# Kernel optimization log

Hardware: AMD Instinct MI355X
Metric: run time of the kernel (lower is better)

## Reference

```python
import jax, jax.numpy as jnp
import numpy as np

NUM_EXPERTS = 8
HIDDEN = 1024
INTERMEDIATE = 2816
TOTAL_TOKENS = 4096  # 512 tokens per expert


def setup_inputs() -> dict:
    key = jax.random.key(0)
    k_x, k1, k2, k3 = jax.random.split(key, 4)
    hiddens = jax.random.normal(k_x, (TOTAL_TOKENS, HIDDEN), dtype=jnp.float32)
    # tokens assumed pre-sorted by expert; equal-sized groups here
    batch_sizes = jnp.full((NUM_EXPERTS,), TOTAL_TOKENS // NUM_EXPERTS, dtype=jnp.int64)
    w1_weight = jax.random.normal(k1, (NUM_EXPERTS, HIDDEN, INTERMEDIATE), dtype=jnp.float32)
    w2_weight = jax.random.normal(k2, (NUM_EXPERTS, INTERMEDIATE, HIDDEN), dtype=jnp.float32)
    w3_weight = jax.random.normal(k3, (NUM_EXPERTS, HIDDEN, INTERMEDIATE), dtype=jnp.float32)
    return {
        "hiddens": hiddens,
        "w1_weight": w1_weight,
        "w2_weight": w2_weight,
        "w3_weight": w3_weight,
        "batch_sizes": batch_sizes,
    }


def _grouped_moe(hiddens, w1, w2, w3, batch_sizes):
    """Grouped SwiGLU FFN: tokens are contiguous per expert (sizes = batch_sizes).

    Jit-safe formulation: map each token to its expert id, then run one masked
    dense GEMM trio per expert (small fixed expert count). Zero rows contribute
    exactly zero (silu(0)*0 == 0), so no final masking of the output is needed.
    """
    num_experts = w1.shape[0]
    total_tokens = hiddens.shape[0]
    bounds = jnp.cumsum(batch_sizes)  # [E] exclusive-right boundaries
    expert_ids = jnp.searchsorted(bounds, jnp.arange(total_tokens), side="right")  # [T]
    out = jnp.zeros((total_tokens, w2.shape[-1]), dtype=hiddens.dtype)
    for e in range(num_experts):
        mask = (expert_ids == e)[:, None]  # [T, 1]
        xe = jnp.where(mask, hiddens, 0)   # zero out other experts' tokens
        up = jax.nn.silu(xe @ w1[e]) * (xe @ w3[e])  # [T, F] SwiGLU
        out = out + up @ w2[e]             # [T, H]
    return out


def reference(hiddens, w1_weight, w2_weight, w3_weight, batch_sizes):
    return _grouped_moe(hiddens, w1_weight, w2_weight, w3_weight, batch_sizes)
```

## Files before the change

### kernel.cpp

```cpp
#include <hip/hip_runtime.h>
#include <hip/hip_bf16.h>

#define NE 8
#define HD 1024
#define ID 2816
#define TT 4096
#define BM 128
#define BK 32
#define BN1 64
#define BN2 64
#define MAXMT (TT / BM + NE)
#define NKS1 (HD / BK)
#define NKS2 (ID / BK)
#define ATILE 8192

typedef __attribute__((ext_vector_type(4))) float f32x4;
typedef __attribute__((ext_vector_type(8))) short s16x8;
typedef __attribute__((ext_vector_type(4))) int i32x4;

__device__ __forceinline__ unsigned int f2bfpk(float lo, float hi) {
  float2 t; t.x = lo; t.y = hi;
  union { __hip_bfloat162 h2; unsigned int u; } cv;
  cv.h2 = __float22bfloat162_rn(t);
  return cv.u;
}

__device__ __forceinline__ void lds_barrier() {
  asm volatile("s_waitcnt lgkmcnt(0)" ::: "memory");
  __builtin_amdgcn_s_barrier();
}

__device__ __forceinline__ void glds16(const void* g, void* l) {
  __builtin_amdgcn_global_load_lds(
      (const __attribute__((address_space(1))) void*)g,
      (__attribute__((address_space(3))) void*)l, 16, 0, 0);
}

__device__ __forceinline__ bool map_tile(const void* bsp, int mt, int& e,
                                         int& mstart, int& rowend) {
  const int* w = (const int*)bsp;
  bool is64 = (w[1] == 0) && (w[3] == 0) && (w[5] == 0) && (w[7] == 0) &&
              ((w[0] | w[2] | w[4] | w[6]) != 0);
  long long start = 0;
  int rem = mt;
  for (int i = 0; i < NE; ++i) {
    long long b = is64 ? ((const long long*)bsp)[i] : (long long)w[i];
    if (b < 0) b = 0;
    int tiles = (int)((b + BM - 1) / BM);
    if (rem < tiles) {
      long long m0 = start + (long long)rem * BM;
      long long me = start + b;
      if (m0 >= TT) return false;
      if (me > TT) me = TT;
      e = i; mstart = (int)m0; rowend = (int)me;
      return true;
    }
    rem -= tiles;
    start += b;
  }
  return false;
}

__global__ __launch_bounds__(256) void cvt_xt(const float* __restrict__ x,
                                              const void* __restrict__ bsp,
                                              unsigned short* __restrict__ xt) {
  int mt = blockIdx.x >> 5;
  int ks = blockIdx.x & 31;
  int e, mstart, rowend;
  if (!map_tile(bsp, mt, e, mstart, rowend)) return;
  int t = threadIdx.x;
  int lane = t & 63;
  int r = lane & 15, q = lane >> 4;
  unsigned short* ob = xt + ((size_t)mt * NKS1 + ks) * (ATILE / 2);
#pragma unroll
  for (int h = 0; h < 2; ++h) {
    int f = h * 4 + (t >> 6);
    int row = mstart + f * 16 + r;
    s16x8 o = (s16x8)0;
    if (row < rowend) {
      const float* src = x + (size_t)row * HD + ks * 32 + q * 8;
      f32x4 v0 = *(const f32x4*)src;
      f32x4 v1 = *(const f32x4*)(src + 4);
      unsigned int d0 = f2bfpk(v0[0], v0[1]), d1 = f2bfpk(v0[2], v0[3]);
      unsigned int d2 = f2bfpk(v1[0], v1[1]), d3 = f2bfpk(v1[2], v1[3]);
      o[0] = (short)d0; o[1] = (short)(d0 >> 16);
      o[2] = (short)d1; o[3] = (short)(d1 >> 16);
      o[4] = (short)d2; o[5] = (short)(d2 >> 16);
      o[6] = (short)d3; o[7] = (short)(d3 >> 16);
    }
    *(s16x8*)(ob + h * 2048 + t * 8) = o;
  }
}

__global__ __launch_bounds__(256, 4) void moe_gemm1(
    const unsigned short* __restrict__ xt, const float* __restrict__ w1,
    const float* __restrict__ w3, const void* __restrict__ bsp,
    __hip_bfloat16* __restrict__ up) {
  __shared__ __align__(16) char As[2][ATILE];
  __shared__ __align__(16) char B1s[2][4096];
  __shared__ __align__(16) char B3s[2][4096];

  const int NWG = (ID / BN1) * MAXMT;
  int bid = blockIdx.x;
  int logical = (bid & 7) * (NWG >> 3) + (bid >> 3);
  int mt = logical % MAXMT;
  int nt = logical / MAXMT;
  int e, mstart, rowend;
  if (!map_tile(bsp, mt, e, mstart, rowend)) return;
  const int n0 = nt * BN1;
  const int tid = threadIdx.x;
  const int lane = tid & 63;
  const int wv = tid >> 6;
  const int wr = wv >> 1, wc = wv & 1;
  const int q = lane >> 4, r16 = lane & 15;

  const int b_n = tid & 63, b_kq = tid >> 6;
  const int boff = (b_n >> 4) * 1024 + b_kq * 256 + (b_n & 15) * 16;
  const char* agp = (const char*)xt + (size_t)mt * NKS1 * ATILE + tid * 16;
  const float* w1c = w1 + (size_t)e * HD * ID + (size_t)(8 * b_kq) * ID + n0 + b_n;
  const float* w3c = w3 + (size_t)e * HD * ID + (size_t)(8 * b_kq) * ID + n0 + b_n;

  f32x4 acc1[4][2], acc3[4][2];
#pragma unroll
  for (int i = 0; i < 4; ++i)
#pragma unroll
    for (int j = 0; j < 2; ++j) { acc1[i][j] = (f32x4)0.f; acc3[i][j] = (f32x4)0.f; }

  float Wc1[8], Wc3[8];

  auto gldsA = [&](int k, int buf) {
    const char* s = agp + (size_t)k * ATILE;
    char* d = &As[buf][0] + tid * 16;
    glds16(s, d);
    glds16(s + 4096, d + 4096);
  };
  auto loadB = [&]() {
#pragma unroll
    for (int i = 0; i < 8; ++i) {
      Wc1[i] = w1c[(size_t)i * ID];
      Wc3[i] = w3c[(size_t)i * ID];
    }
    w1c += (size_t)BK * ID; w3c += (size_t)BK * ID;
  };
  auto storeB = [&](int buf) {
    i32x4 p1, p3;
    p1[0] = (int)f2bfpk(Wc1[0], Wc1[1]); p1[1] = (int)f2bfpk(Wc1[2], Wc1[3]);
    p1[2] = (int)f2bfpk(Wc1[4], Wc1[5]); p1[3] = (int)f2bfpk(Wc1[6], Wc1[7]);
    *(i32x4*)(B1s[buf] + boff) = p1;
    p3[0] = (int)f2bfpk(Wc3[0], Wc3[1]); p3[1] = (int)f2bfpk(Wc3[2], Wc3[3]);
    p3[2] = (int)f2bfpk(Wc3[4], Wc3[5]); p3[3] = (int)f2bfpk(Wc3[6], Wc3[7]);
    *(i32x4*)(B3s[buf] + boff) = p3;
  };
  auto compute = [&](int ab, int bb) {
    s16x8 a[4], b1[2], b3[2];
#pragma unroll
    for (int i = 0; i < 4; ++i)
      a[i] = *(const s16x8*)(As[ab] + (wr * 4 + i) * 1024 + lane * 16);
#pragma unroll
    for (int j = 0; j < 2; ++j) {
      b1[j] = *(const s16x8*)(B1s[bb] + (wc * 2 + j) * 1024 + lane * 16);
      b3[j] = *(const s16x8*)(B3s[bb] + (wc * 2 + j) * 1024 + lane * 16);
    }
#pragma unroll
    for (int i = 0; i < 4; ++i)
#pragma unroll
      for (int j = 0; j < 2; ++j) {
        acc1[i][j] = __builtin_amdgcn_mfma_f32_16x16x32_bf16(a[i], b1[j], acc1[i][j], 0, 0, 0);
        acc3[i][j] = __builtin_amdgcn_mfma_f32_16x16x32_bf16(a[i], b3[j], acc3[i][j], 0, 0, 0);
      }
  };

  gldsA(0, 0);
  __builtin_amdgcn_sched_barrier(0);
  loadB();
  storeB(0);
  lds_barrier();
  for (int kt = 0; kt < NKS1; kt += 2) {
    if (kt + 1 < NKS1) {
      gldsA(kt + 1, 1);
      __builtin_amdgcn_sched_barrier(0);
      loadB();
      __builtin_amdgcn_sched_barrier(0);
    }
    compute(0, 0);
    if (kt + 1 < NKS1) { storeB(1); lds_barrier(); }
    if (kt + 2 < NKS1) {
      gldsA(kt + 2, 0);
      __builtin_amdgcn_sched_barrier(0);
      loadB();
      __builtin_amdgcn_sched_barrier(0);
    }
    compute(1, 1);
    if (kt + 2 < NKS1) { storeB(0); lds_barrier(); }
  }

#pragma unroll
  for (int i = 0; i < 4; ++i)
#pragma unroll
    for (int r = 0; r < 4; ++r) {
      int gm = mstart + wr * 64 + i * 16 + q * 4 + r;
      if (gm < rowend) {
#pragma unroll
        for (int j = 0; j < 2; ++j) {
          float v1 = acc1[i][j][r], v3 = acc3[i][j][r];
          float s = v1 / (1.f + __expf(-v1));
          up[(size_t)gm * ID + n0 + wc * 32 + j * 16 + r16] = __float2bfloat16(s * v3);
        }
      }
    }
}

__global__ __launch_bounds__(256, 4) void moe_gemm2(
    const __hip_bfloat16* __restrict__ up, const float* __restrict__ w2,
    const void* __restrict__ bsp, float* __restrict__ out) {
  __shared__ __align__(16) char As[2][ATILE];
  __shared__ __align__(16) char Bs[2][4096];

  const int NWG = (HD / BN2) * MAXMT;
  int bid = blockIdx.x;
  int logical = (bid & 7) * (NWG >> 3) + (bid >> 3);
  int mt = logical % MAXMT;
  int nt = logical / MAXMT;
  int e, mstart, rowend;
  if (!map_tile(bsp, mt, e, mstart, rowend)) return;
  const int n0 = nt * BN2;
  const int tid = threadIdx.x;
  const int lane = tid & 63;
  const int wv = tid >> 6;
  const int wr = wv >> 1, wc = wv & 1;
  const int q = lane >> 4, r16 = lane & 15;

  const int b_n = tid & 63, b_kq = tid >> 6;
  const int boff = (b_n >> 4) * 1024 + b_kq * 256 + (b_n & 15) * 16;
  const float* w2c = w2 + (size_t)e * ID * HD + (size_t)(8 * b_kq) * HD + n0 + b_n;

  int row0 = mstart + (tid >> 6) * 16 + (tid & 15);
  int row1 = row0 + 64;
  row0 = row0 < TT ? row0 : TT - 1;
  row1 = row1 < TT ? row1 : TT - 1;
  const char* uc0 = (const char*)up + ((size_t)row0 * ID + q * 8) * 2;
  const char* uc1 = (const char*)up + ((size_t)row1 * ID + q * 8) * 2;

  f32x4 acc[4][2];
#pragma unroll
  for (int i = 0; i < 4; ++i)
#pragma unroll
    for (int j = 0; j < 2; ++j) acc[i][j] = (f32x4)0.f;

  float Wc[8];

  auto gldsA = [&](int buf) {
    char* d = &As[buf][0] + tid * 16;
    glds16(uc0, d);
    glds16(uc1, d + 4096);
    uc0 += BK * 2; uc1 += BK * 2;
  };
  auto loadB = [&]() {
#pragma unroll
    for (int i = 0; i < 8; ++i) Wc[i] = w2c[(size_t)i * HD];
    w2c += (size_t)BK * HD;
  };
  auto storeB = [&](int buf) {
    i32x4 p;
    p[0] = (int)f2bfpk(Wc[0], Wc[1]); p[1] = (int)f2bfpk(Wc[2], Wc[3]);
    p[2] = (int)f2bfpk(Wc[4], Wc[5]); p[3] = (int)f2bfpk(Wc[6], Wc[7]);
    *(i32x4*)(Bs[buf] + boff) = p;
  };
  auto compute = [&](int ab, int bb) {
    s16x8 a[4], b[2];
#pragma unroll
    for (int i = 0; i < 4; ++i)
      a[i] = *(const s16x8*)(As[ab] + (wr * 4 + i) * 1024 + lane * 16);
#pragma unroll
    for (int j = 0; j < 2; ++j)
      b[j] = *(const s16x8*)(Bs[bb] + (wc * 2 + j) * 1024 + lane * 16);
#pragma unroll
    for (int i = 0; i < 4; ++i)
#pragma unroll
      for (int j = 0; j < 2; ++j)
        acc[i][j] = __builtin_amdgcn_mfma_f32_16x16x32_bf16(a[i], b[j], acc[i][j], 0, 0, 0);
  };

  gldsA(0);
  __builtin_amdgcn_sched_barrier(0);
  loadB();
  storeB(0);
  lds_barrier();
  for (int kt = 0; kt < NKS2; kt += 2) {
    if (kt + 1 < NKS2) {
      gldsA(1);
      __builtin_amdgcn_sched_barrier(0);
      loadB();
      __builtin_amdgcn_sched_barrier(0);
    }
    compute(0, 0);
    if (kt + 1 < NKS2) { storeB(1); lds_barrier(); }
    if (kt + 2 < NKS2) {
      gldsA(0);
      __builtin_amdgcn_sched_barrier(0);
      loadB();
      __builtin_amdgcn_sched_barrier(0);
    }
    compute(1, 1);
    if (kt + 2 < NKS2) { storeB(0); lds_barrier(); }
  }

#pragma unroll
  for (int i = 0; i < 4; ++i)
#pragma unroll
    for (int r = 0; r < 4; ++r) {
      int gm = mstart + wr * 64 + i * 16 + q * 4 + r;
      if (gm < rowend) {
#pragma unroll
        for (int j = 0; j < 2; ++j)
          out[(size_t)gm * HD + n0 + wc * 32 + j * 16 + r16] = acc[i][j][r];
      }
    }
}

extern "C" void kernel_launch(void* const* d_in, const int* in_sizes, int n_in,
                              void* d_out, int out_size, void* d_ws, size_t ws_size,
                              hipStream_t stream) {
  const float* x = (const float*)d_in[0];
  const float* w1 = (const float*)d_in[1];
  const float* w2 = (const float*)d_in[2];
  const float* w3 = (const float*)d_in[3];
  const void* bs = d_in[4];
  float* out = (float*)d_out;
  unsigned short* xt = (unsigned short*)d_ws;
  __hip_bfloat16* up =
      (__hip_bfloat16*)((char*)d_ws + (size_t)MAXMT * NKS1 * ATILE);

  hipMemsetAsync(d_out, 0, (size_t)out_size * sizeof(float), stream);

  cvt_xt<<<dim3(MAXMT * NKS1), dim3(256), 0, stream>>>(x, bs, xt);
  moe_gemm1<<<dim3((ID / BN1) * MAXMT), dim3(256), 0, stream>>>(xt, w1, w3, bs, up);
  moe_gemm2<<<dim3((HD / BN2) * MAXMT), dim3(256), 0, stream>>>(up, w2, bs, out);
}
```

Before: 205.2 us.

## Prefetch weight tiles two stages ahead with register double-buffering and partial vmcnt waits

Both GEMM kernels now keep two register buffers for the fp32 weight tile, so global loads for stage k+2 are issued before computing stage k. Barriers use explicit s_waitcnt vmcnt(N) to wait only for older loads, letting the newest weight loads stay in flight across the barrier. This hides more global-memory latency on the weight stream. The cost is more registers, so gemm1 launch bounds drop from 4 to 3 waves per SIMD, which lowers occupancy, and correctness depends on the hand-counted vmcnt values.

```diff
diff --git a/kernel.cpp b/kernel.cpp
--- a/kernel.cpp
+++ b/kernel.cpp
@@ -23,11 +23,6 @@
   union { __hip_bfloat162 h2; unsigned int u; } cv;
   cv.h2 = __float22bfloat162_rn(t);
   return cv.u;
-}
-
-__device__ __forceinline__ void lds_barrier() {
-  asm volatile("s_waitcnt lgkmcnt(0)" ::: "memory");
-  __builtin_amdgcn_s_barrier();
 }
 
 __device__ __forceinline__ void glds16(const void* g, void* l) {
@@ -92,7 +87,7 @@
   }
 }
 
-__global__ __launch_bounds__(256, 4) void moe_gemm1(
+__global__ __launch_bounds__(256, 3) void moe_gemm1(
     const unsigned short* __restrict__ xt, const float* __restrict__ w1,
     const float* __restrict__ w3, const void* __restrict__ bsp,
     __hip_bfloat16* __restrict__ up) {
@@ -126,7 +121,7 @@
 #pragma unroll
     for (int j = 0; j < 2; ++j) { acc1[i][j] = (f32x4)0.f; acc3[i][j] = (f32x4)0.f; }
 
-  float Wc1[8], Wc3[8];
+  float Wa1[8], Wa3[8], Wb1[8], Wb3[8];
 
   auto gldsA = [&](int k, int buf) {
     const char* s = agp + (size_t)k * ATILE;
@@ -134,21 +129,21 @@
     glds16(s, d);
     glds16(s + 4096, d + 4096);
   };
-  auto loadB = [&]() {
+  auto loadB = [&](float* W1_, float* W3_) {
 #pragma unroll
     for (int i = 0; i < 8; ++i) {
-      Wc1[i] = w1c[(size_t)i * ID];
-      Wc3[i] = w3c[(size_t)i * ID];
+      W1_[i] = w1c[(size_t)i * ID];
+      W3_[i] = w3c[(size_t)i * ID];
     }
     w1c += (size_t)BK * ID; w3c += (size_t)BK * ID;
   };
-  auto storeB = [&](int buf) {
+  auto storeB = [&](int buf, const float* W1_, const float* W3_) {
     i32x4 p1, p3;
-    p1[0] = (int)f2bfpk(Wc1[0], Wc1[1]); p1[1] = (int)f2bfpk(Wc1[2], Wc1[3]);
-    p1[2] = (int)f2bfpk(Wc1[4], Wc1[5]); p1[3] = (int)f2bfpk(Wc1[6], Wc1[7]);
+    p1[0] = (int)f2bfpk(W1_[0], W1_[1]); p1[1] = (int)f2bfpk(W1_[2], W1_[3]);
+    p1[2] = (int)f2bfpk(W1_[4], W1_[5]); p1[3] = (int)f2bfpk(W1_[6], W1_[7]);
     *(i32x4*)(B1s[buf] + boff) = p1;
-    p3[0] = (int)f2bfpk(Wc3[0], Wc3[1]); p3[1] = (int)f2bfpk(Wc3[2], Wc3[3]);
-    p3[2] = (int)f2bfpk(Wc3[4], Wc3[5]); p3[3] = (int)f2bfpk(Wc3[6], Wc3[7]);
+    p3[0] = (int)f2bfpk(W3_[0], W3_[1]); p3[1] = (int)f2bfpk(W3_[2], W3_[3]);
+    p3[2] = (int)f2bfpk(W3_[4], W3_[5]); p3[3] = (int)f2bfpk(W3_[6], W3_[7]);
     *(i32x4*)(B3s[buf] + boff) = p3;
   };
   auto compute = [&](int ab, int bb) {
@@ -170,29 +165,43 @@
       }
   };
 
+#define G1PHASE(P, KC)                                                    \
+  {                                                                       \
+    const bool doG = (kt + (KC) + 1 < NKS1);                              \
+    const bool doL = (kt + (KC) + 2 < NKS1);                              \
+    if (doG) {                                                            \
+      gldsA(kt + (KC) + 1, (P) ^ 1);                                      \
+      __builtin_amdgcn_sched_barrier(0);                                  \
+    }                                                                     \
+    if (doL) {                                                            \
+      loadB((P) ? Wb1 : Wa1, (P) ? Wb3 : Wa3);                            \
+      __builtin_amdgcn_sched_barrier(0);                                  \
+    }                                                                     \
+    compute((P), (P));                                                    \
+    if (doG) {                                                            \
+      storeB((P) ^ 1, (P) ? Wa1 : Wb1, (P) ? Wa3 : Wb3);                  \
+      if (doL)                                                            \
+        asm volatile("s_waitcnt vmcnt(16) lgkmcnt(0)" ::: "memory");      \
+      else                                                                \
+        asm volatile("s_waitcnt vmcnt(0) lgkmcnt(0)" ::: "memory");       \
+      __builtin_amdgcn_s_barrier();                                       \
+    }                                                                     \
+  }
+
   gldsA(0, 0);
   __builtin_amdgcn_sched_barrier(0);
-  loadB();
-  storeB(0);
-  lds_barrier();
+  loadB(Wa1, Wa3);
+  __builtin_amdgcn_sched_barrier(0);
+  loadB(Wb1, Wb3);
+  storeB(0, Wa1, Wa3);
+  asm volatile("s_waitcnt vmcnt(16) lgkmcnt(0)" ::: "memory");
+  __builtin_amdgcn_s_barrier();
+
   for (int kt = 0; kt < NKS1; kt += 2) {
-    if (kt + 1 < NKS1) {
-      gldsA(kt + 1, 1);
-      __builtin_amdgcn_sched_barrier(0);
-      loadB();
-      __builtin_amdgcn_sched_barrier(0);
-    }
-    compute(0, 0);
-    if (kt + 1 < NKS1) { storeB(1); lds_barrier(); }
-    if (kt + 2 < NKS1) {
-      gldsA(kt + 2, 0);
-      __builtin_amdgcn_sched_barrier(0);
-      loadB();
-      __builtin_amdgcn_sched_barrier(0);
-    }
-    compute(1, 1);
-    if (kt + 2 < NKS1) { storeB(0); lds_barrier(); }
-  }
+    G1PHASE(0, 0)
+    G1PHASE(1, 1)
+  }
+#undef G1PHASE
 
 #pragma unroll
   for (int i = 0; i < 4; ++i)
@@ -247,7 +256,7 @@
 #pragma unroll
     for (int j = 0; j < 2; ++j) acc[i][j] = (f32x4)0.f;
 
-  float Wc[8];
+  float Wa[8], Wb[8];
 
   auto gldsA = [&](int buf) {
     char* d = &As[buf][0] + tid * 16;
@@ -255,15 +264,15 @@
     glds16(uc1, d + 4096);
     uc0 += BK * 2; uc1 += BK * 2;
   };
-  auto loadB = [&]() {
-#pragma unroll
-    for (int i = 0; i < 8; ++i) Wc[i] = w2c[(size_t)i * HD];
+  auto loadB = [&](float* W_) {
+#pragma unroll
+    for (int i = 0; i < 8; ++i) W_[i] = w2c[(size_t)i * HD];
     w2c += (size_t)BK * HD;
   };
-  auto storeB = [&](int buf) {
+  auto storeB = [&](int buf, const float* W_) {
     i32x4 p;
-    p[0] = (int)f2bfpk(Wc[0], Wc[1]); p[1] = (int)f2bfpk(Wc[2], Wc[3]);
-    p[2] = (int)f2bfpk(Wc[4], Wc[5]); p[3] = (int)f2bfpk(Wc[6], Wc[7]);
+    p[0] = (int)f2bfpk(W_[0], W_[1]); p[1] = (int)f2bfpk(W_[2], W_[3]);
+    p[2] = (int)f2bfpk(W_[4], W_[5]); p[3] = (int)f2bfpk(W_[6], W_[7]);
     *(i32x4*)(Bs[buf] + boff) = p;
   };
   auto compute = [&](int ab, int bb) {
@@ -281,29 +290,43 @@
         acc[i][j] = __builtin_amdgcn_mfma_f32_16x16x32_bf16(a[i], b[j], acc[i][j], 0, 0, 0);
   };
 
+#define G2PHASE(P, KC)                                                    \
+  {                                                                       \
+    const bool doG = (kt + (KC) + 1 < NKS2);                              \
+    const bool doL = (kt + (KC) + 2 < NKS2);                              \
+    if (doG) {                                                            \
+      gldsA((P) ^ 1);                                                     \
+      __builtin_amdgcn_sched_barrier(0);                                  \
+    }                                                                     \
+    if (doL) {                                                            \
+      loadB((P) ? Wb : Wa);                                               \
+      __builtin_amdgcn_sched_barrier(0);                                  \
+    }                                                                     \
+    compute((P), (P));                                                    \
+    if (doG) {                                                            \
+      storeB((P) ^ 1, (P) ? Wa : Wb);                                     \
+      if (doL)                                                            \
+        asm volatile("s_waitcnt vmcnt(8) lgkmcnt(0)" ::: "memory");       \
+      else                                                                \
+        asm volatile("s_waitcnt vmcnt(0) lgkmcnt(0)" ::: "memory");       \
+      __builtin_amdgcn_s_barrier();                                       \
+    }                                                                     \
+  }
+
   gldsA(0);
   __builtin_amdgcn_sched_barrier(0);
-  loadB();
-  storeB(0);
-  lds_barrier();
+  loadB(Wa);
+  __builtin_amdgcn_sched_barrier(0);
+  loadB(Wb);
+  storeB(0, Wa);
+  asm volatile("s_waitcnt vmcnt(8) lgkmcnt(0)" ::: "memory");
+  __builtin_amdgcn_s_barrier();
+
   for (int kt = 0; kt < NKS2; kt += 2) {
-    if (kt + 1 < NKS2) {
-      gldsA(1);
-      __builtin_amdgcn_sched_barrier(0);
-      loadB();
-      __builtin_amdgcn_sched_barrier(0);
-    }
-    compute(0, 0);
-    if (kt + 1 < NKS2) { storeB(1); lds_barrier(); }
-    if (kt + 2 < NKS2) {
-      gldsA(0);
-      __builtin_amdgcn_sched_barrier(0);
-      loadB();
-      __builtin_amdgcn_sched_barrier(0);
-    }
-    compute(1, 1);
-    if (kt + 2 < NKS2) { storeB(0); lds_barrier(); }
-  }
+    G2PHASE(0, 0)
+    G2PHASE(1, 1)
+  }
+#undef G2PHASE
 
 #pragma unroll
   for (int i = 0; i < 4; ++i)
```

New measurement: 206.5 us. Within noise of the previous version (+0.7%).
